# Kernel tuning notes

Measured on AMD Instinct MI355X. Metric: run time of the kernel, lower is better.

The kernel has to match this reference:

```python
import jax, jax.numpy as jnp
import numpy as np

N = 50000
E = 800000
C_IN = 32
C_OUT = 32
K = 8  # number of branch MLPs


def setup_inputs() -> dict:
    key = jax.random.key(0)
    ks = jax.random.split(key, 12)
    x = jax.random.normal(ks[0], (N, C_IN), dtype=jnp.float32)
    pos = jax.random.normal(ks[1], (N, 2), dtype=jnp.float32)
    edge_index = jax.random.randint(ks[2], (2, E), 0, N, dtype=jnp.int32)
    edge_attr = jax.random.normal(ks[3], (E, 4), dtype=jnp.float32)
    edge_weight = jax.random.uniform(ks[4], (E,), dtype=jnp.float32)
    s1 = 1.0 / np.sqrt(C_IN + 4)
    s2 = 1.0 / np.sqrt(C_OUT)
    W1 = jax.random.uniform(ks[5], (K, C_IN + 4, C_OUT), jnp.float32, -s1, s1)
    b1 = jax.random.uniform(ks[6], (K, C_OUT), jnp.float32, -s1, s1)
    W2 = jax.random.uniform(ks[7], (K, C_OUT, C_OUT), jnp.float32, -s2, s2)
    b2 = jax.random.uniform(ks[8], (K, C_OUT), jnp.float32, -s2, s2)
    sr = 1.0 / np.sqrt(C_IN)
    Wr = jax.random.uniform(ks[9], (C_IN, C_OUT), jnp.float32, -sr, sr)
    br = jax.random.uniform(ks[10], (C_OUT,), jnp.float32, -sr, sr)
    return {"x": x, "pos": pos, "edge_index": edge_index, "edge_attr": edge_attr,
            "edge_weight": edge_weight, "W1": W1, "b1": b1, "W2": W2, "b2": b2,
            "Wr": Wr, "br": br}


def reference(x, pos, edge_index, edge_attr, edge_weight, W1, b1, W2, b2, Wr, br):
    src = edge_index[0]  # j (source / neighbor)
    tgt = edge_index[1]  # i (target / aggregation index)

    # gather per-edge features
    x_i = x[tgt]                      # [E, C_IN]
    x_j = x[src]                      # [E, C_IN]
    diff = pos[src] - pos[tgt]        # [E, 2]

    # geometric branch index in [0, 8)
    con0 = (diff[:, 0] > 0).astype(jnp.int32)
    con1 = (diff[:, 1] > 0).astype(jnp.int32)
    con2 = (jnp.abs(diff[:, 0]) - jnp.abs(diff[:, 1]) > 0).astype(jnp.int32)
    idx = con0 + con1 * 2 + con2 * 4  # [E]

    m = jnp.concatenate([x_j - x_i, edge_attr], axis=1)  # [E, C_IN+4]
    # all 8 branch MLPs (Linear->ReLU->Linear->ReLU), then select per edge
    h = jax.nn.relu(jnp.einsum('ec,kcf->ekf', m, W1) + b1[None])   # [E, K, C_OUT]
    f_all = jax.nn.relu(jnp.einsum('ekf,kfg->ekg', h, W2) + b2[None])
    f = jnp.take_along_axis(f_all, idx[:, None, None], axis=1)[:, 0, :]  # [E, C_OUT]
    f = edge_weight[:, None] * f

    # scatter-mean over target nodes
    seg_sum = jax.ops.segment_sum(f, tgt, num_segments=N)
    counts = jax.ops.segment_sum(jnp.ones((f.shape[0],), f.dtype), tgt, num_segments=N)
    out = seg_sum / jnp.maximum(counts, 1.0)[:, None]

    # skip connection
    out = out + x @ Wr + br
    return out
```

## Files before the change

kernel.cpp:

```cpp
#include <hip/hip_runtime.h>

#define N_NODES 50000
#define N_EDGES 800000
#define K_BR    8
#define BCAP    131072
#define MLP_SLOTS (K_BR * BCAP)
#define SCAN_BLOCKS 196

typedef _Float16 h2 __attribute__((ext_vector_type(2)));
typedef _Float16 half8 __attribute__((ext_vector_type(8)));
typedef float f32x4 __attribute__((ext_vector_type(4)));

#define MFMA(a, b, c) __builtin_amdgcn_mfma_f32_16x16x32_f16((a), (b), (c), 0, 0, 0)

#define VAL_MASK 0x3FFFFFFFu
#define FLG_A    0x40000000u
#define FLG_P    0x80000000u


__device__ __forceinline__ int branch_idx(float dx, float dy) {
    return (dx > 0.0f ? 1 : 0) + (dy > 0.0f ? 2 : 0) +
           ((fabsf(dx) - fabsf(dy)) > 0.0f ? 4 : 0);
}

__device__ __forceinline__ unsigned pk_f16pair(float a, float b) {
    h2 p; p.x = (_Float16)a; p.y = (_Float16)b;
    return __builtin_bit_cast(unsigned, p);
}

__device__ __forceinline__ unsigned short f16bits(float a) {
    _Float16 h = (_Float16)a;
    return __builtin_bit_cast(unsigned short, h);
}

__global__ void pass1_kernel(const int* __restrict__ ei, const float* __restrict__ pos,
                             const float* __restrict__ ea, const float* __restrict__ ew,
                             const float* __restrict__ x,
                             const float* __restrict__ W1, const float* __restrict__ W2,
                             int* __restrict__ cnt, int* __restrict__ bucketCur,
                             uint4* __restrict__ payload, unsigned* __restrict__ xh,
                             uint4* __restrict__ w1f4, uint4* __restrict__ w2f4) {
    __shared__ int h[K_BR];
    __shared__ int base[K_BR];
    int t = threadIdx.x;
    int e = blockIdx.x * 256 + t;
    if (t < K_BR) h[t] = 0;
    __syncthreads();

    int s = ei[e], d = ei[N_EDGES + e];
    float2 ps = ((const float2*)pos)[s];
    float2 pd = ((const float2*)pos)[d];
    int k = branch_idx(ps.x - pd.x, ps.y - pd.y);
    int rank = atomicAdd(&h[k], 1);
    __syncthreads();
    if (t < K_BR) base[t] = (h[t] > 0) ? atomicAdd(&bucketCur[t], h[t]) : 0;
    __syncthreads();

    int slotLocal = atomicAdd(&cnt[d], 1);
    float4 eav = ((const float4*)ea)[e];
    unsigned ewh = (unsigned)f16bits(ew[e]);

    float2 xv = ((const float2*)x)[e];
    xh[e] = pk_f16pair(xv.x, xv.y);

    if (e < 2048) {
        int L = e & 63, fl = e >> 6;
        int nt = fl & 1, kt = (fl >> 1) & 1, kk = fl >> 2;
        int quad = L >> 4, col = L & 15;
        unsigned dw[4];
#pragma unroll
        for (int i = 0; i < 4; ++i) {
            float v0 = 0.0f, v1 = 0.0f;
            int k0 = kt * 32 + quad * 8 + 2 * i;
            if (k0 < 36)     v0 = W1[kk * 1152 + k0 * 32 + nt * 16 + col];
            if (k0 + 1 < 36) v1 = W1[kk * 1152 + (k0 + 1) * 32 + nt * 16 + col];
            dw[i] = pk_f16pair(v0, v1);
        }
        w1f4[e] = make_uint4(dw[0], dw[1], dw[2], dw[3]);
    } else if (e < 3072) {
        int u2 = e - 2048;
        int L = u2 & 63, fl = u2 >> 6;
        int nt = fl & 1, kk = fl >> 1;
        int quad = L >> 4, col = L & 15;
        unsigned dw[4];
#pragma unroll
        for (int i = 0; i < 4; ++i) {
            int k0 = quad * 8 + 2 * i;
            dw[i] = pk_f16pair(W2[kk * 1024 + k0 * 32 + nt * 16 + col],
                               W2[kk * 1024 + (k0 + 1) * 32 + nt * 16 + col]);
        }
        w2f4[u2] = make_uint4(dw[0], dw[1], dw[2], dw[3]);
    }

    int idx = (k << 17) + base[k] + rank;
    payload[idx] = make_uint4((unsigned)s | ((unsigned)d << 16),
                              (unsigned)slotLocal | (ewh << 16),
                              pk_f16pair(eav.x, eav.y),
                              pk_f16pair(eav.z, eav.w));
}

__global__ void scan_kernel(const int* __restrict__ cnt, unsigned* __restrict__ ps,
                            int* __restrict__ nodeStart) {
    __shared__ int s[256];
    __shared__ int sh_off;
    int t = threadIdx.x, b = blockIdx.x;
    int i = b * 256 + t;
    int v = (i < N_NODES) ? cnt[i] : 0;
    s[t] = v;
    __syncthreads();
#pragma unroll
    for (int off = 1; off < 256; off <<= 1) {
        int tmp = (t >= off) ? s[t - off] : 0;
        __syncthreads();
        s[t] += tmp;
        __syncthreads();
    }
    int excl = s[t] - v;
    if (t == 255)
        atomicExch(&ps[b], (unsigned)s[255] | (b == 0 ? FLG_P : FLG_A));
    if (t == 0) sh_off = 0;
    if (t < 64 && b > 0) {
        int off = 0;
        int base = b - 1;
        for (;;) {
            int idx = base - t;
            unsigned w = 0;
            if (idx >= 0) {
                do { w = atomicOr(&ps[idx], 0u); } while (!(w & (FLG_A | FLG_P)));
            }
            bool isP = (w & FLG_P) != 0;
            unsigned long long pm = __ballot(isP);
            int firstP = pm ? (__ffsll((unsigned long long)pm) - 1) : 64;
            int contrib = (idx >= 0 && t <= firstP) ? (int)(w & VAL_MASK) : 0;
#pragma unroll
            for (int sh = 32; sh > 0; sh >>= 1) contrib += __shfl_down(contrib, sh, 64);
            contrib = __shfl(contrib, 0, 64);
            off += contrib;
            if (firstP < 64 || base - 64 < 0) break;
            base -= 64;
        }
        if (t == 0) sh_off = off;
    }
    __syncthreads();
    if (i < N_NODES) nodeStart[i] = excl + sh_off;
}

__global__ void __launch_bounds__(64) mlp_kernel(
    const uint4* __restrict__ payload,
    const unsigned* __restrict__ xh,
    const uint4* __restrict__ w1f4, const float* __restrict__ b1,
    const uint4* __restrict__ w2f4, const float* __restrict__ b2,
    const int* __restrict__ nodeStart,
    const int* __restrict__ bucketFill,
    unsigned short* __restrict__ fbuf) {
    __shared__ uint4 lds4[656];
    char* mreg = (char*)lds4;
    char* hreg = mreg + 9216;

    int t = blockIdx.x * 64 + threadIdx.x;
    int u = __builtin_amdgcn_readfirstlane(t);
    int k = u >> 17;
    int fill = bucketFill[k];
    if ((u & (BCAP - 1)) >= fill) return;
    int rel = t & (BCAP - 1);
    bool valid = rel < fill;
    int idx = (k << 17) + min(rel, fill - 1);

    int L = threadIdx.x;
    int quad = L >> 4, col = L & 15;

    uint4 pl = payload[idx];
    int s = (int)(pl.x & 0xFFFFu);
    int d = (int)(pl.x >> 16);
    _Float16 wh = __builtin_bit_cast(_Float16, (unsigned short)(pl.y >> 16));
    int slot = valid ? (nodeStart[d] + (int)(pl.y & 0xFFFFu)) : 0;

    const uint4* xj = ((const uint4*)xh) + 4 * (size_t)s;
    const uint4* xi = ((const uint4*)xh) + 4 * (size_t)d;
    uint4* mrow = (uint4*)(mreg + L * 144);
#pragma unroll
    for (int q = 0; q < 4; ++q) {
        half8 a8 = __builtin_bit_cast(half8, xj[q]);
        half8 b8 = __builtin_bit_cast(half8, xi[q]);
        half8 d8 = a8 - b8;
        mrow[q] = __builtin_bit_cast(uint4, d8);
    }
    mrow[4] = make_uint4(pl.z, pl.w, 0u, 0u);
    mrow[5] = make_uint4(0u, 0u, 0u, 0u);
    mrow[6] = make_uint4(0u, 0u, 0u, 0u);
    mrow[7] = make_uint4(0u, 0u, 0u, 0u);

    half8 B1[2][2], B2[2];
#pragma unroll
    for (int kt = 0; kt < 2; ++kt)
#pragma unroll
        for (int nt = 0; nt < 2; ++nt)
            B1[kt][nt] = __builtin_bit_cast(half8, w1f4[((k * 2 + kt) * 2 + nt) * 64 + L]);
#pragma unroll
    for (int nt = 0; nt < 2; ++nt)
        B2[nt] = __builtin_bit_cast(half8, w2f4[(k * 2 + nt) * 64 + L]);
    float b1o0 = b1[k * 32 + col],      b1o1 = b1[k * 32 + 16 + col];
    float b2o0 = b2[k * 32 + col],      b2o1 = b2[k * 32 + 16 + col];

#pragma unroll
    for (int mt = 0; mt < 4; ++mt) {
        int arow = mt * 16 + col;
        half8 a0 = __builtin_bit_cast(half8, *(const uint4*)(mreg + arow * 144 + quad * 16));
        half8 a1 = __builtin_bit_cast(half8, *(const uint4*)(mreg + arow * 144 + 64 + quad * 16));
        f32x4 c0 = {b1o0, b1o0, b1o0, b1o0};
        f32x4 c1 = {b1o1, b1o1, b1o1, b1o1};
        c0 = MFMA(a0, B1[0][0], c0);
        c0 = MFMA(a1, B1[1][0], c0);
        c1 = MFMA(a0, B1[0][1], c1);
        c1 = MFMA(a1, B1[1][1], c1);
#pragma unroll
        for (int r = 0; r < 4; ++r) {
            int er = quad * 4 + r;
            *(unsigned short*)(hreg + er * 80 + col * 2)        = f16bits(fmaxf(c0[r], 0.0f));
            *(unsigned short*)(hreg + er * 80 + (16 + col) * 2) = f16bits(fmaxf(c1[r], 0.0f));
        }
        half8 ah = __builtin_bit_cast(half8, *(const uint4*)(hreg + col * 80 + quad * 16));
        f32x4 d0 = {b2o0, b2o0, b2o0, b2o0};
        f32x4 d1 = {b2o1, b2o1, b2o1, b2o1};
        d0 = MFMA(ah, B2[0], d0);
        d1 = MFMA(ah, B2[1], d1);
#pragma unroll
        for (int r = 0; r < 4; ++r) {
            int edge = mt * 16 + quad * 4 + r;
            *(unsigned short*)(mreg + edge * 144 + col * 2)        = f16bits(fmaxf(d0[r], 0.0f));
            *(unsigned short*)(mreg + edge * 144 + (16 + col) * 2) = f16bits(fmaxf(d1[r], 0.0f));
        }
    }

    half8 w8 = {wh, wh, wh, wh, wh, wh, wh, wh};
    uint4* orow = (uint4*)(mreg + L * 144);
    uint4* frow = (uint4*)(fbuf + 32 * (size_t)slot);
#pragma unroll
    for (int q = 0; q < 4; ++q) {
        half8 v8 = __builtin_bit_cast(half8, orow[q]);
        v8 = v8 * w8;
        if (valid) frow[q] = __builtin_bit_cast(uint4, v8);
    }
}

__global__ void agg_kernel(const unsigned short* __restrict__ fbuf,
                           const int* __restrict__ nodeStart, const int* __restrict__ deg,
                           const float* __restrict__ x, const float* __restrict__ Wr,
                           const float* __restrict__ br, float* __restrict__ out) {
    int t = blockIdx.x * blockDim.x + threadIdx.x;
    if (t >= N_NODES * 8) return;
    int n = t >> 3, g8 = t & 7;
    int st = nodeStart[n], dg = deg[n];
    const uint2* fb = (const uint2*)fbuf;
    float a0 = 0.0f, a1 = 0.0f, a2 = 0.0f, a3 = 0.0f;
    for (int j = 0; j < dg; ++j) {
        uint2 uu = fb[(size_t)(st + j) * 8 + g8];
        h2 p01 = __builtin_bit_cast(h2, uu.x);
        h2 p23 = __builtin_bit_cast(h2, uu.y);
        a0 += (float)p01.x;
        a1 += (float)p01.y;
        a2 += (float)p23.x;
        a3 += (float)p23.y;
    }
    float inv = 1.0f / (float)max(dg, 1);
    int o = g8 * 4;
    a0 = a0 * inv + br[o];
    a1 = a1 * inv + br[o + 1];
    a2 = a2 * inv + br[o + 2];
    a3 = a3 * inv + br[o + 3];
    const float* xr = x + 32 * (size_t)n;
#pragma unroll
    for (int c = 0; c < 32; ++c) {
        float xv = xr[c];
        a0 = fmaf(xv, Wr[c * 32 + o], a0);
        a1 = fmaf(xv, Wr[c * 32 + o + 1], a1);
        a2 = fmaf(xv, Wr[c * 32 + o + 2], a2);
        a3 = fmaf(xv, Wr[c * 32 + o + 3], a3);
    }
    float4* o4 = (float4*)(out + 32 * (size_t)n + o);
    *o4 = make_float4(a0, a1, a2, a3);
}

extern "C" void kernel_launch(void* const* d_in, const int* in_sizes, int n_in,
                              void* d_out, int out_size, void* d_ws, size_t ws_size,
                              hipStream_t stream) {
    const float* x   = (const float*)d_in[0];
    const float* pos = (const float*)d_in[1];
    const int*   ei  = (const int*)d_in[2];
    const float* ea  = (const float*)d_in[3];
    const float* ew  = (const float*)d_in[4];
    const float* W1  = (const float*)d_in[5];
    const float* b1  = (const float*)d_in[6];
    const float* W2  = (const float*)d_in[7];
    const float* b2  = (const float*)d_in[8];
    const float* Wr  = (const float*)d_in[9];
    const float* br  = (const float*)d_in[10];
    float* out = (float*)d_out;

    char* ws = (char*)d_ws;
    unsigned short* fbuf = (unsigned short*)(ws + 0);
    uint4* payload  = (uint4*)(ws + 51200000);
    int* cnt        = (int*)(ws + 67977216);
    int* bucketCur  = (int*)(ws + 68177216);
    unsigned* psLb  = (unsigned*)(ws + 68177248);
    int* nodeStart  = (int*)(ws + 68178048);
    uint4* w1f4     = (uint4*)(ws + 68378048);
    uint4* w2f4     = (uint4*)(ws + 68410816);
    unsigned* xh    = (unsigned*)(ws + 68427200);

    hipMemsetAsync(cnt, 0, 200832, stream);

    pass1_kernel<<<N_EDGES / 256, 256, 0, stream>>>(ei, pos, ea, ew, x, W1, W2,
                                                    cnt, bucketCur, payload, xh,
                                                    w1f4, w2f4);
    scan_kernel<<<SCAN_BLOCKS, 256, 0, stream>>>(cnt, psLb, nodeStart);
    mlp_kernel<<<MLP_SLOTS / 64, 64, 0, stream>>>(payload, xh, w1f4, b1, w2f4, b2,
                                                  nodeStart, bucketCur, fbuf);
    agg_kernel<<<(N_NODES * 8 + 255) / 256, 256, 0, stream>>>(fbuf, nodeStart, cnt,
                                                              x, Wr, br, out);
}
```

Before: 200.4 us.

## Privatize per-node edge counters per XCC to avoid cross-die atomics

The per-destination degree counter is split into eight copies indexed by the hardware XCC id read from a register, and the atomic increments use workgroup scope instead of device scope. The scan sums the eight copies, writes the total degree and a per-XCC base offset, and the MLP kernel computes each edge's output slot from that base plus the local rank. This aims to keep counter atomics in the local die's L2 rather than paying coherent cross-XCC traffic. In exchange the memset and counter memory grow eightfold, and it relies on workgroup-scope atomics staying correct among blocks on the same XCC.

New measurement: 210.0 us. 4.8% more time.

```diff
diff --git a/kernel.cpp b/kernel.cpp
--- a/kernel.cpp
+++ b/kernel.cpp
@@ -33,11 +33,15 @@
     return __builtin_bit_cast(unsigned short, h);
 }
 
+__device__ __forceinline__ int xcc_id() {
+    return (int)(__builtin_amdgcn_s_getreg((31 << 11) | 20) & 7u);
+}
+
 __global__ void pass1_kernel(const int* __restrict__ ei, const float* __restrict__ pos,
                              const float* __restrict__ ea, const float* __restrict__ ew,
                              const float* __restrict__ x,
                              const float* __restrict__ W1, const float* __restrict__ W2,
-                             int* __restrict__ cnt, int* __restrict__ bucketCur,
+                             int* __restrict__ cntX, int* __restrict__ bucketCur,
                              uint4* __restrict__ payload, unsigned* __restrict__ xh,
                              uint4* __restrict__ w1f4, uint4* __restrict__ w2f4) {
     __shared__ int h[K_BR];
@@ -56,7 +60,9 @@
     if (t < K_BR) base[t] = (h[t] > 0) ? atomicAdd(&bucketCur[t], h[t]) : 0;
     __syncthreads();
 
-    int slotLocal = atomicAdd(&cnt[d], 1);
+    int xc = xcc_id();
+    int rk = __hip_atomic_fetch_add(&cntX[xc * N_NODES + d], 1,
+                                    __ATOMIC_RELAXED, __HIP_MEMORY_SCOPE_WORKGROUP);
     float4 eav = ((const float4*)ea)[e];
     unsigned ewh = (unsigned)f16bits(ew[e]);
 
@@ -94,18 +100,27 @@
 
     int idx = (k << 17) + base[k] + rank;
     payload[idx] = make_uint4((unsigned)s | ((unsigned)d << 16),
-                              (unsigned)slotLocal | (ewh << 16),
+                              (unsigned)rk | ((unsigned)xc << 8) | (ewh << 16),
                               pk_f16pair(eav.x, eav.y),
                               pk_f16pair(eav.z, eav.w));
 }
 
-__global__ void scan_kernel(const int* __restrict__ cnt, unsigned* __restrict__ ps,
-                            int* __restrict__ nodeStart) {
+__global__ void scan_kernel(const int* __restrict__ cntX, unsigned* __restrict__ ps,
+                            int* __restrict__ nodeStart, int* __restrict__ deg,
+                            int* __restrict__ baseX) {
     __shared__ int s[256];
     __shared__ int sh_off;
     int t = threadIdx.x, b = blockIdx.x;
     int i = b * 256 + t;
-    int v = (i < N_NODES) ? cnt[i] : 0;
+    int c[8];
+    int v = 0;
+    if (i < N_NODES) {
+#pragma unroll
+        for (int xx = 0; xx < 8; ++xx) { c[xx] = cntX[xx * N_NODES + i]; v += c[xx]; }
+    } else {
+#pragma unroll
+        for (int xx = 0; xx < 8; ++xx) c[xx] = 0;
+    }
     s[t] = v;
     __syncthreads();
 #pragma unroll
@@ -142,7 +157,14 @@
         if (t == 0) sh_off = off;
     }
     __syncthreads();
-    if (i < N_NODES) nodeStart[i] = excl + sh_off;
+    if (i < N_NODES) {
+        int ns = excl + sh_off;
+        nodeStart[i] = ns;
+        deg[i] = v;
+        int run = ns;
+#pragma unroll
+        for (int xx = 0; xx < 8; ++xx) { baseX[xx * N_NODES + i] = run; run += c[xx]; }
+    }
 }
 
 __global__ void __launch_bounds__(64) mlp_kernel(
@@ -150,7 +172,7 @@
     const unsigned* __restrict__ xh,
     const uint4* __restrict__ w1f4, const float* __restrict__ b1,
     const uint4* __restrict__ w2f4, const float* __restrict__ b2,
-    const int* __restrict__ nodeStart,
+    const int* __restrict__ baseX,
     const int* __restrict__ bucketFill,
     unsigned short* __restrict__ fbuf) {
     __shared__ uint4 lds4[656];
@@ -173,7 +195,9 @@
     int s = (int)(pl.x & 0xFFFFu);
     int d = (int)(pl.x >> 16);
     _Float16 wh = __builtin_bit_cast(_Float16, (unsigned short)(pl.y >> 16));
-    int slot = valid ? (nodeStart[d] + (int)(pl.y & 0xFFFFu)) : 0;
+    int rk = (int)(pl.y & 0xFFu);
+    int xc = (int)((pl.y >> 8) & 7u);
+    int slot = valid ? (baseX[xc * N_NODES + d] + rk) : 0;
 
     const uint4* xj = ((const uint4*)xh) + 4 * (size_t)s;
     const uint4* xi = ((const uint4*)xh) + 4 * (size_t)d;
@@ -300,22 +324,24 @@
     char* ws = (char*)d_ws;
     unsigned short* fbuf = (unsigned short*)(ws + 0);
     uint4* payload  = (uint4*)(ws + 51200000);
-    int* cnt        = (int*)(ws + 67977216);
-    int* bucketCur  = (int*)(ws + 68177216);
-    unsigned* psLb  = (unsigned*)(ws + 68177248);
-    int* nodeStart  = (int*)(ws + 68178048);
-    uint4* w1f4     = (uint4*)(ws + 68378048);
-    uint4* w2f4     = (uint4*)(ws + 68410816);
-    unsigned* xh    = (unsigned*)(ws + 68427200);
-
-    hipMemsetAsync(cnt, 0, 200832, stream);
+    int* cntX       = (int*)(ws + 67977216);
+    int* bucketCur  = (int*)(ws + 69577216);
+    unsigned* psLb  = (unsigned*)(ws + 69577248);
+    int* deg        = (int*)(ws + 69578048);
+    int* nodeStart  = (int*)(ws + 69778048);
+    int* baseX      = (int*)(ws + 69978048);
+    uint4* w1f4     = (uint4*)(ws + 71578048);
+    uint4* w2f4     = (uint4*)(ws + 71610816);
+    unsigned* xh    = (unsigned*)(ws + 71627200);
+
+    hipMemsetAsync(cntX, 0, 1600832, stream);
 
     pass1_kernel<<<N_EDGES / 256, 256, 0, stream>>>(ei, pos, ea, ew, x, W1, W2,
-                                                    cnt, bucketCur, payload, xh,
+                                                    cntX, bucketCur, payload, xh,
                                                     w1f4, w2f4);
-    scan_kernel<<<SCAN_BLOCKS, 256, 0, stream>>>(cnt, psLb, nodeStart);
+    scan_kernel<<<SCAN_BLOCKS, 256, 0, stream>>>(cntX, psLb, nodeStart, deg, baseX);
     mlp_kernel<<<MLP_SLOTS / 64, 64, 0, stream>>>(payload, xh, w1f4, b1, w2f4, b2,
-                                                  nodeStart, bucketCur, fbuf);
-    agg_kernel<<<(N_NODES * 8 + 255) / 256, 256, 0, stream>>>(fbuf, nodeStart, cnt,
+                                                  baseX, bucketCur, fbuf);
+    agg_kernel<<<(N_NODES * 8 + 255) / 256, 256, 0, stream>>>(fbuf, nodeStart, deg,
                                                               x, Wr, br, out);
 }
```

## Bucket edges by branch and target-node chunk, aggregate in LDS per chunk

Applied to the files above, without the earlier changes.

Replaces the per-node counting sort and decoupled-lookback scan with a two-pass bucket sort keyed by (branch, 256-node chunk). Each bucket is padded to a multiple of 64 so MLP waves stay branch-uniform. Aggregation runs one block per node chunk, accumulating into LDS with shared atomics instead of reading a per-node contiguous segment. This removes the global per-node atomics and the scan, but adds an extra pass over the edges, one single-block prefix kernel, and heavy contention on LDS atomics.

Result: slower. 359.2 us (+79.2%).

```diff
diff --git a/kernel.cpp b/kernel.cpp
--- a/kernel.cpp
+++ b/kernel.cpp
@@ -3,9 +3,11 @@
 #define N_NODES 50000
 #define N_EDGES 800000
 #define K_BR    8
-#define BCAP    131072
-#define MLP_SLOTS (K_BR * BCAP)
-#define SCAN_BLOCKS 196
+#define N_C     196
+#define N_BUK   1568
+#define CAP_SLOTS 898816
+#define MLP_WAVES (CAP_SLOTS/64)
+#define FATB    98
 
 typedef _Float16 h2 __attribute__((ext_vector_type(2)));
 typedef _Float16 half8 __attribute__((ext_vector_type(8)));
@@ -13,10 +15,6 @@
 
 #define MFMA(a, b, c) __builtin_amdgcn_mfma_f32_16x16x32_f16((a), (b), (c), 0, 0, 0)
 
-#define VAL_MASK 0x3FFFFFFFu
-#define FLG_A    0x40000000u
-#define FLG_P    0x80000000u
-
 
 __device__ __forceinline__ int branch_idx(float dx, float dy) {
     return (dx > 0.0f ? 1 : 0) + (dy > 0.0f ? 2 : 0) +
@@ -33,116 +31,134 @@
     return __builtin_bit_cast(unsigned short, h);
 }
 
-__global__ void pass1_kernel(const int* __restrict__ ei, const float* __restrict__ pos,
-                             const float* __restrict__ ea, const float* __restrict__ ew,
-                             const float* __restrict__ x,
-                             const float* __restrict__ W1, const float* __restrict__ W2,
-                             int* __restrict__ cnt, int* __restrict__ bucketCur,
-                             uint4* __restrict__ payload, unsigned* __restrict__ xh,
-                             uint4* __restrict__ w1f4, uint4* __restrict__ w2f4) {
-    __shared__ int h[K_BR];
-    __shared__ int base[K_BR];
+__global__ void __launch_bounds__(1024) hist_kernel(
+    const int* __restrict__ ei, const float* __restrict__ pos,
+    const float* __restrict__ x,
+    int* __restrict__ bucketCnt, unsigned short* __restrict__ kcArr,
+    unsigned* __restrict__ xh) {
+    __shared__ int h[N_BUK];
     int t = threadIdx.x;
-    int e = blockIdx.x * 256 + t;
-    if (t < K_BR) h[t] = 0;
-    __syncthreads();
-
-    int s = ei[e], d = ei[N_EDGES + e];
-    float2 ps = ((const float2*)pos)[s];
-    float2 pd = ((const float2*)pos)[d];
-    int k = branch_idx(ps.x - pd.x, ps.y - pd.y);
-    int rank = atomicAdd(&h[k], 1);
-    __syncthreads();
-    if (t < K_BR) base[t] = (h[t] > 0) ? atomicAdd(&bucketCur[t], h[t]) : 0;
-    __syncthreads();
-
-    int slotLocal = atomicAdd(&cnt[d], 1);
-    float4 eav = ((const float4*)ea)[e];
-    unsigned ewh = (unsigned)f16bits(ew[e]);
-
-    float2 xv = ((const float2*)x)[e];
-    xh[e] = pk_f16pair(xv.x, xv.y);
-
-    if (e < 2048) {
-        int L = e & 63, fl = e >> 6;
-        int nt = fl & 1, kt = (fl >> 1) & 1, kk = fl >> 2;
-        int quad = L >> 4, col = L & 15;
-        unsigned dw[4];
-#pragma unroll
-        for (int i = 0; i < 4; ++i) {
-            float v0 = 0.0f, v1 = 0.0f;
-            int k0 = kt * 32 + quad * 8 + 2 * i;
-            if (k0 < 36)     v0 = W1[kk * 1152 + k0 * 32 + nt * 16 + col];
-            if (k0 + 1 < 36) v1 = W1[kk * 1152 + (k0 + 1) * 32 + nt * 16 + col];
-            dw[i] = pk_f16pair(v0, v1);
-        }
-        w1f4[e] = make_uint4(dw[0], dw[1], dw[2], dw[3]);
-    } else if (e < 3072) {
-        int u2 = e - 2048;
-        int L = u2 & 63, fl = u2 >> 6;
-        int nt = fl & 1, kk = fl >> 1;
-        int quad = L >> 4, col = L & 15;
-        unsigned dw[4];
-#pragma unroll
-        for (int i = 0; i < 4; ++i) {
-            int k0 = quad * 8 + 2 * i;
-            dw[i] = pk_f16pair(W2[kk * 1024 + k0 * 32 + nt * 16 + col],
-                               W2[kk * 1024 + (k0 + 1) * 32 + nt * 16 + col]);
-        }
-        w2f4[u2] = make_uint4(dw[0], dw[1], dw[2], dw[3]);
-    }
-
-    int idx = (k << 17) + base[k] + rank;
-    payload[idx] = make_uint4((unsigned)s | ((unsigned)d << 16),
-                              (unsigned)slotLocal | (ewh << 16),
-                              pk_f16pair(eav.x, eav.y),
-                              pk_f16pair(eav.z, eav.w));
-}
-
-__global__ void scan_kernel(const int* __restrict__ cnt, unsigned* __restrict__ ps,
-                            int* __restrict__ nodeStart) {
-    __shared__ int s[256];
-    __shared__ int sh_off;
-    int t = threadIdx.x, b = blockIdx.x;
-    int i = b * 256 + t;
-    int v = (i < N_NODES) ? cnt[i] : 0;
-    s[t] = v;
-    __syncthreads();
-#pragma unroll
-    for (int off = 1; off < 256; off <<= 1) {
-        int tmp = (t >= off) ? s[t - off] : 0;
+    for (int j = t; j < N_BUK; j += 1024) h[j] = 0;
+    __syncthreads();
+#pragma unroll
+    for (int i = 0; i < 8; ++i) {
+        int e = blockIdx.x * 8192 + i * 1024 + t;
+        if (e < N_EDGES) {
+            int s = ei[e], d = ei[N_EDGES + e];
+            float2 ps = ((const float2*)pos)[s];
+            float2 pd = ((const float2*)pos)[d];
+            int k = branch_idx(ps.x - pd.x, ps.y - pd.y);
+            int b = k * N_C + (d >> 8);
+            atomicAdd(&h[b], 1);
+            kcArr[e] = (unsigned short)b;
+            float2 xv = ((const float2*)x)[e];
+            xh[e] = pk_f16pair(xv.x, xv.y);
+        }
+    }
+    __syncthreads();
+    for (int j = t; j < N_BUK; j += 1024) {
+        int c = h[j];
+        if (c) atomicAdd(&bucketCnt[j], c);
+    }
+}
+
+__global__ void __launch_bounds__(1024) tiny_kernel(
+    const int* __restrict__ bucketCnt, int* __restrict__ slotStart,
+    const float* __restrict__ W1, const float* __restrict__ W2,
+    uint4* __restrict__ w1f4, uint4* __restrict__ w2f4) {
+    __shared__ int sc[1024];
+    int t = threadIdx.x;
+    int b0 = 2 * t, b1 = 2 * t + 1;
+    int a0 = (b0 < N_BUK) ? ((bucketCnt[b0] + 63) & ~63) : 0;
+    int a1 = (b1 < N_BUK) ? ((bucketCnt[b1] + 63) & ~63) : 0;
+    sc[t] = a0 + a1;
+    __syncthreads();
+    for (int off = 1; off < 1024; off <<= 1) {
+        int tmp = (t >= off) ? sc[t - off] : 0;
         __syncthreads();
-        s[t] += tmp;
+        sc[t] += tmp;
         __syncthreads();
     }
-    int excl = s[t] - v;
-    if (t == 255)
-        atomicExch(&ps[b], (unsigned)s[255] | (b == 0 ? FLG_P : FLG_A));
-    if (t == 0) sh_off = 0;
-    if (t < 64 && b > 0) {
-        int off = 0;
-        int base = b - 1;
-        for (;;) {
-            int idx = base - t;
-            unsigned w = 0;
-            if (idx >= 0) {
-                do { w = atomicOr(&ps[idx], 0u); } while (!(w & (FLG_A | FLG_P)));
+    int excl = sc[t] - (a0 + a1);
+    if (b0 < N_BUK) slotStart[b0] = excl;
+    if (b1 < N_BUK) slotStart[b1] = excl + a0;
+    if (t == 1023) slotStart[N_BUK] = sc[1023];
+
+    for (int idx = t; idx < 3072; idx += 1024) {
+        if (idx < 2048) {
+            int L = idx & 63, fl = idx >> 6;
+            int nt = fl & 1, kt = (fl >> 1) & 1, kk = fl >> 2;
+            int quad = L >> 4, col = L & 15;
+            unsigned dw[4];
+#pragma unroll
+            for (int i = 0; i < 4; ++i) {
+                float v0 = 0.0f, v1 = 0.0f;
+                int k0 = kt * 32 + quad * 8 + 2 * i;
+                if (k0 < 36)     v0 = W1[kk * 1152 + k0 * 32 + nt * 16 + col];
+                if (k0 + 1 < 36) v1 = W1[kk * 1152 + (k0 + 1) * 32 + nt * 16 + col];
+                dw[i] = pk_f16pair(v0, v1);
             }
-            bool isP = (w & FLG_P) != 0;
-            unsigned long long pm = __ballot(isP);
-            int firstP = pm ? (__ffsll((unsigned long long)pm) - 1) : 64;
-            int contrib = (idx >= 0 && t <= firstP) ? (int)(w & VAL_MASK) : 0;
-#pragma unroll
-            for (int sh = 32; sh > 0; sh >>= 1) contrib += __shfl_down(contrib, sh, 64);
-            contrib = __shfl(contrib, 0, 64);
-            off += contrib;
-            if (firstP < 64 || base - 64 < 0) break;
-            base -= 64;
-        }
-        if (t == 0) sh_off = off;
-    }
-    __syncthreads();
-    if (i < N_NODES) nodeStart[i] = excl + sh_off;
+            w1f4[idx] = make_uint4(dw[0], dw[1], dw[2], dw[3]);
+        } else {
+            int u2 = idx - 2048;
+            int L = u2 & 63, fl = u2 >> 6;
+            int nt = fl & 1, kk = fl >> 1;
+            int quad = L >> 4, col = L & 15;
+            unsigned dw[4];
+#pragma unroll
+            for (int i = 0; i < 4; ++i) {
+                int k0 = quad * 8 + 2 * i;
+                dw[i] = pk_f16pair(W2[kk * 1024 + k0 * 32 + nt * 16 + col],
+                                   W2[kk * 1024 + (k0 + 1) * 32 + nt * 16 + col]);
+            }
+            w2f4[u2] = make_uint4(dw[0], dw[1], dw[2], dw[3]);
+        }
+    }
+}
+
+__global__ void __launch_bounds__(1024) scatter_kernel(
+    const int* __restrict__ ei, const float* __restrict__ ea,
+    const float* __restrict__ ew, const unsigned short* __restrict__ kcArr,
+    const int* __restrict__ slotStart, int* __restrict__ bucketCur,
+    uint4* __restrict__ payload) {
+    __shared__ int h[N_BUK];
+    __shared__ int base[N_BUK];
+    int t = threadIdx.x;
+    for (int j = t; j < N_BUK; j += 1024) h[j] = 0;
+    __syncthreads();
+    unsigned sd[8], brk[8], e01[8], e23[8], ewh[8];
+#pragma unroll
+    for (int i = 0; i < 8; ++i) {
+        int e = blockIdx.x * 8192 + i * 1024 + t;
+        bool v = e < N_EDGES;
+        int b = 0, rk = 0;
+        if (v) {
+            int s = ei[e], d = ei[N_EDGES + e];
+            sd[i] = (unsigned)s | ((unsigned)d << 16);
+            b = kcArr[e];
+            rk = atomicAdd(&h[b], 1);
+            float4 eav = ((const float4*)ea)[e];
+            e01[i] = pk_f16pair(eav.x, eav.y);
+            e23[i] = pk_f16pair(eav.z, eav.w);
+            ewh[i] = (unsigned)f16bits(ew[e]);
+        }
+        brk[i] = (unsigned)b | ((unsigned)rk << 16) | (v ? 0x80000000u : 0u);
+    }
+    __syncthreads();
+    for (int j = t; j < N_BUK; j += 1024) {
+        int c = h[j];
+        base[j] = c ? atomicAdd(&bucketCur[j], c) : 0;
+    }
+    __syncthreads();
+#pragma unroll
+    for (int i = 0; i < 8; ++i) {
+        if (brk[i] & 0x80000000u) {
+            int b = (int)(brk[i] & 0xFFFFu);
+            int rk = (int)((brk[i] >> 16) & 0x7FFFu);
+            int slot = slotStart[b] + base[b] + rk;
+            payload[slot] = make_uint4(sd[i], ewh[i] << 16, e01[i], e23[i]);
+        }
+    }
 }
 
 __global__ void __launch_bounds__(64) mlp_kernel(
@@ -150,30 +166,35 @@
     const unsigned* __restrict__ xh,
     const uint4* __restrict__ w1f4, const float* __restrict__ b1,
     const uint4* __restrict__ w2f4, const float* __restrict__ b2,
-    const int* __restrict__ nodeStart,
-    const int* __restrict__ bucketFill,
+    const int* __restrict__ slotStart, const int* __restrict__ bucketCnt,
     unsigned short* __restrict__ fbuf) {
     __shared__ uint4 lds4[656];
     char* mreg = (char*)lds4;
     char* hreg = mreg + 9216;
 
-    int t = blockIdx.x * 64 + threadIdx.x;
-    int u = __builtin_amdgcn_readfirstlane(t);
-    int k = u >> 17;
-    int fill = bucketFill[k];
-    if ((u & (BCAP - 1)) >= fill) return;
-    int rel = t & (BCAP - 1);
-    bool valid = rel < fill;
-    int idx = (k << 17) + min(rel, fill - 1);
+    int u = __builtin_amdgcn_readfirstlane((int)blockIdx.x * 64);
+    if (u >= slotStart[N_BUK]) return;
+    int lo = 0;
+#pragma unroll
+    for (int st = 1024; st; st >>= 1) {
+        int cand = lo + st;
+        if (cand < N_BUK && slotStart[cand] <= u) lo = cand;
+    }
+    int b = __builtin_amdgcn_readfirstlane(lo);
+    int fill = bucketCnt[b];
+    int rel0 = u - slotStart[b];
+    if (rel0 >= fill) return;
+    int k = b / N_C;
 
     int L = threadIdx.x;
     int quad = L >> 4, col = L & 15;
-
-    uint4 pl = payload[idx];
+    int slot = u + L;
+    bool valid = (rel0 + L) < fill;
+
+    uint4 pl = payload[slot];
     int s = (int)(pl.x & 0xFFFFu);
     int d = (int)(pl.x >> 16);
     _Float16 wh = __builtin_bit_cast(_Float16, (unsigned short)(pl.y >> 16));
-    int slot = valid ? (nodeStart[d] + (int)(pl.y & 0xFFFFu)) : 0;
 
     const uint4* xj = ((const uint4*)xh) + 4 * (size_t)s;
     const uint4* xi = ((const uint4*)xh) + 4 * (size_t)d;
@@ -216,8 +237,10 @@
 #pragma unroll
         for (int r = 0; r < 4; ++r) {
             int er = quad * 4 + r;
-            *(unsigned short*)(hreg + er * 80 + col * 2)        = f16bits(fmaxf(c0[r], 0.0f));
-            *(unsigned short*)(hreg + er * 80 + (16 + col) * 2) = f16bits(fmaxf(c1[r], 0.0f));
+            *(unsigned short*)(hreg + er * 80 + col * 2) =
+                __builtin_bit_cast(unsigned short, (_Float16)fmaxf(c0[r], 0.0f));
+            *(unsigned short*)(hreg + er * 80 + (16 + col) * 2) =
+                __builtin_bit_cast(unsigned short, (_Float16)fmaxf(c1[r], 0.0f));
         }
         half8 ah = __builtin_bit_cast(half8, *(const uint4*)(hreg + col * 80 + quad * 16));
         f32x4 d0 = {b2o0, b2o0, b2o0, b2o0};
@@ -227,8 +250,10 @@
 #pragma unroll
         for (int r = 0; r < 4; ++r) {
             int edge = mt * 16 + quad * 4 + r;
-            *(unsigned short*)(mreg + edge * 144 + col * 2)        = f16bits(fmaxf(d0[r], 0.0f));
-            *(unsigned short*)(mreg + edge * 144 + (16 + col) * 2) = f16bits(fmaxf(d1[r], 0.0f));
+            *(unsigned short*)(mreg + edge * 144 + col * 2) =
+                __builtin_bit_cast(unsigned short, (_Float16)fmaxf(d0[r], 0.0f));
+            *(unsigned short*)(mreg + edge * 144 + (16 + col) * 2) =
+                __builtin_bit_cast(unsigned short, (_Float16)fmaxf(d1[r], 0.0f));
         }
     }
 
@@ -243,42 +268,50 @@
     }
 }
 
-__global__ void agg_kernel(const unsigned short* __restrict__ fbuf,
-                           const int* __restrict__ nodeStart, const int* __restrict__ deg,
-                           const float* __restrict__ x, const float* __restrict__ Wr,
-                           const float* __restrict__ br, float* __restrict__ out) {
-    int t = blockIdx.x * blockDim.x + threadIdx.x;
-    if (t >= N_NODES * 8) return;
-    int n = t >> 3, g8 = t & 7;
-    int st = nodeStart[n], dg = deg[n];
-    const uint2* fb = (const uint2*)fbuf;
-    float a0 = 0.0f, a1 = 0.0f, a2 = 0.0f, a3 = 0.0f;
-    for (int j = 0; j < dg; ++j) {
-        uint2 uu = fb[(size_t)(st + j) * 8 + g8];
-        h2 p01 = __builtin_bit_cast(h2, uu.x);
-        h2 p23 = __builtin_bit_cast(h2, uu.y);
-        a0 += (float)p01.x;
-        a1 += (float)p01.y;
-        a2 += (float)p23.x;
-        a3 += (float)p23.y;
-    }
-    float inv = 1.0f / (float)max(dg, 1);
-    int o = g8 * 4;
-    a0 = a0 * inv + br[o];
-    a1 = a1 * inv + br[o + 1];
-    a2 = a2 * inv + br[o + 2];
-    a3 = a3 * inv + br[o + 3];
-    const float* xr = x + 32 * (size_t)n;
-#pragma unroll
-    for (int c = 0; c < 32; ++c) {
-        float xv = xr[c];
-        a0 = fmaf(xv, Wr[c * 32 + o], a0);
-        a1 = fmaf(xv, Wr[c * 32 + o + 1], a1);
-        a2 = fmaf(xv, Wr[c * 32 + o + 2], a2);
-        a3 = fmaf(xv, Wr[c * 32 + o + 3], a3);
-    }
-    float4* o4 = (float4*)(out + 32 * (size_t)n + o);
-    *o4 = make_float4(a0, a1, a2, a3);
+__global__ void __launch_bounds__(1024) agg_kernel(
+    const unsigned short* __restrict__ fbuf, const uint4* __restrict__ payload,
+    const int* __restrict__ slotStart, const int* __restrict__ bucketCnt,
+    const float* __restrict__ x, const float* __restrict__ Wr,
+    const float* __restrict__ br, float* __restrict__ out) {
+    __shared__ float acc[8192];
+    __shared__ int cntN[256];
+    int t = threadIdx.x, c = blockIdx.x;
+    for (int j = t; j < 8192; j += 1024) acc[j] = 0.0f;
+    if (t < 256) cntN[t] = 0;
+    __syncthreads();
+    int r8 = t >> 3, lane = t & 7;
+    for (int k = 0; k < K_BR; ++k) {
+        int b = k * N_C + c;
+        int st = slotStart[b], rows = bucketCnt[b];
+        for (int base = 0; base < rows; base += 128) {
+            int r = base + r8;
+            if (r < rows) {
+                int slot = st + r;
+                int n = (int)(payload[slot].x >> 16) & 255;
+                uint2 v = ((const uint2*)fbuf)[(size_t)slot * 8 + lane];
+                h2 p01 = __builtin_bit_cast(h2, v.x);
+                h2 p23 = __builtin_bit_cast(h2, v.y);
+                int ch = lane * 4;
+                atomicAdd(&acc[n * 32 + ch + 0], (float)p01.x);
+                atomicAdd(&acc[n * 32 + ch + 1], (float)p01.y);
+                atomicAdd(&acc[n * 32 + ch + 2], (float)p23.x);
+                atomicAdd(&acc[n * 32 + ch + 3], (float)p23.y);
+                if (lane == 0) atomicAdd(&cntN[n], 1);
+            }
+        }
+    }
+    __syncthreads();
+    for (int j = t; j < 8192; j += 1024) {
+        int n = j >> 5, ch = j & 31;
+        int g = c * 256 + n;
+        if (g < N_NODES) {
+            float a = acc[j] / (float)max(cntN[n], 1) + br[ch];
+            const float* xr = x + 32 * (size_t)g;
+#pragma unroll
+            for (int cc = 0; cc < 32; ++cc) a = fmaf(xr[cc], Wr[cc * 32 + ch], a);
+            out[(size_t)g * 32 + ch] = a;
+        }
+    }
 }
 
 extern "C" void kernel_launch(void* const* d_in, const int* in_sizes, int n_in,
@@ -298,24 +331,24 @@
     float* out = (float*)d_out;
 
     char* ws = (char*)d_ws;
-    unsigned short* fbuf = (unsigned short*)(ws + 0);
-    uint4* payload  = (uint4*)(ws + 51200000);
-    int* cnt        = (int*)(ws + 67977216);
-    int* bucketCur  = (int*)(ws + 68177216);
-    unsigned* psLb  = (unsigned*)(ws + 68177248);
-    int* nodeStart  = (int*)(ws + 68178048);
-    uint4* w1f4     = (uint4*)(ws + 68378048);
-    uint4* w2f4     = (uint4*)(ws + 68410816);
-    unsigned* xh    = (unsigned*)(ws + 68427200);
-
-    hipMemsetAsync(cnt, 0, 200832, stream);
-
-    pass1_kernel<<<N_EDGES / 256, 256, 0, stream>>>(ei, pos, ea, ew, x, W1, W2,
-                                                    cnt, bucketCur, payload, xh,
-                                                    w1f4, w2f4);
-    scan_kernel<<<SCAN_BLOCKS, 256, 0, stream>>>(cnt, psLb, nodeStart);
-    mlp_kernel<<<MLP_SLOTS / 64, 64, 0, stream>>>(payload, xh, w1f4, b1, w2f4, b2,
-                                                  nodeStart, bucketCur, fbuf);
-    agg_kernel<<<(N_NODES * 8 + 255) / 256, 256, 0, stream>>>(fbuf, nodeStart, cnt,
-                                                              x, Wr, br, out);
-}
+    unsigned short* fbuf   = (unsigned short*)(ws + 0);
+    uint4* payload         = (uint4*)(ws + 57524224);
+    unsigned* xh           = (unsigned*)(ws + 71905280);
+    unsigned short* kcArr  = (unsigned short*)(ws + 75105280);
+    int* bucketCnt         = (int*)(ws + 76705280);
+    int* bucketCur         = (int*)(ws + 76711552);
+    int* slotStart         = (int*)(ws + 76717824);
+    uint4* w1f4            = (uint4*)(ws + 76724224);
+    uint4* w2f4            = (uint4*)(ws + 76756992);
+
+    hipMemsetAsync(bucketCnt, 0, 12544, stream);
+
+    hist_kernel<<<FATB, 1024, 0, stream>>>(ei, pos, x, bucketCnt, kcArr, xh);
+    tiny_kernel<<<1, 1024, 0, stream>>>(bucketCnt, slotStart, W1, W2, w1f4, w2f4);
+    scatter_kernel<<<FATB, 1024, 0, stream>>>(ei, ea, ew, kcArr, slotStart,
+                                              bucketCur, payload);
+    mlp_kernel<<<MLP_WAVES, 64, 0, stream>>>(payload, xh, w1f4, b1, w2f4, b2,
+                                             slotStart, bucketCnt, fbuf);
+    agg_kernel<<<N_C, 1024, 0, stream>>>(fbuf, payload, slotStart, bucketCnt,
+                                         x, Wr, br, out);
+}
```
